# Kernel tuning notes

Measured on AMD Instinct MI355X. Metric: run time of the kernel, lower is better.

The kernel has to match this reference:

```python
import jax, jax.numpy as jnp
import numpy as np
import math

# dims
B, T, HFEAT, E = 32, 8, 128, 128
NUM_CLS, NUM_GLOBAL = 4, 2
NSP = NUM_CLS + NUM_GLOBAL            # 6 special tokens
SCALES = (1, 4, 8)
WINDOW = 4
NHEAD = 8
DH = E // NHEAD                        # 16
NLAYERS = 2                            # blocks per scale = ceil(6/3)
NS = len(SCALES)
F = 512                                # dim_feedforward
ROPE_BASE = 100000.0
NEG = -1e9


def setup_inputs() -> dict:
    key = jax.random.key(0)
    ks = jax.random.split(key, 16)
    def rn(k, shape, s=0.02):
        return jax.random.normal(k, shape, jnp.float32) * s
    inp = {
        'embeddings': jax.random.normal(ks[0], (B, T, NSP + HFEAT, E), jnp.float32),
        'cls_tokens': rn(ks[1], (NUM_CLS, E)),
        'global_tokens': rn(ks[2], (NUM_GLOBAL, E)),
        'Wq': rn(ks[3], (NS, NLAYERS, E, E)),
        'bq': jnp.zeros((NS, NLAYERS, E), jnp.float32),
        'Wk': rn(ks[4], (NS, NLAYERS, E, E)),
        'bk': jnp.zeros((NS, NLAYERS, E), jnp.float32),
        'Wv': rn(ks[5], (NS, NLAYERS, E, E)),
        'bv': jnp.zeros((NS, NLAYERS, E), jnp.float32),
        'Wo': rn(ks[6], (NS, NLAYERS, E, E)),
        'bo': jnp.zeros((NS, NLAYERS, E), jnp.float32),
        'ln1_g': jnp.ones((NS, NLAYERS, E), jnp.float32),
        'ln1_b': jnp.zeros((NS, NLAYERS, E), jnp.float32),
        'ln2_g': jnp.ones((NS, NLAYERS, E), jnp.float32),
        'ln2_b': jnp.zeros((NS, NLAYERS, E), jnp.float32),
        'W1': rn(ks[7], (NS, NLAYERS, E, F)),
        'b1': jnp.zeros((NS, NLAYERS, F), jnp.float32),
        'W2': rn(ks[8], (NS, NLAYERS, F, E)),
        'b2': jnp.zeros((NS, NLAYERS, E), jnp.float32),
        'out_g': jnp.ones((E,), jnp.float32),
        'out_b': jnp.zeros((E,), jnp.float32),
    }
    return inp


def _layernorm(x, g, b, eps=1e-5):
    mu = x.mean(-1, keepdims=True)
    var = ((x - mu) ** 2).mean(-1, keepdims=True)
    return (x - mu) * jax.lax.rsqrt(var + eps) * g + b


def _rope(x):
    # x: (BT, L, H, DH); rotate-half RoPE over head dim
    L = x.shape[1]
    half = DH // 2
    inv = ROPE_BASE ** (-jnp.arange(half, dtype=jnp.float32) / half)
    ang = jnp.arange(L, dtype=jnp.float32)[:, None] * inv[None, :]   # (L, half)
    cos = jnp.cos(ang)[None, :, None, :]
    sin = jnp.sin(ang)[None, :, None, :]
    x1, x2 = x[..., :half], x[..., half:]
    return jnp.concatenate([x1 * cos - x2 * sin, x1 * sin + x2 * cos], axis=-1)


def _sparse_bias(L):
    # global(first NSP) rows/cols fully connected, others window +-WINDOW, diag allowed
    i = jnp.arange(L)
    allowed = (jnp.abs(i[:, None] - i[None, :]) <= WINDOW) | (i[:, None] < NSP) | (i[None, :] < NSP)
    return jnp.where(allowed, 0.0, NEG).astype(jnp.float32)  # (L, L) additive


def _encoder(x, s, Wq, bq, Wk, bk, Wv, bv, Wo, bo, ln1_g, ln1_b, ln2_g, ln2_b, W1, b1, W2, b2, bias):
    # x: (BT, L, E); pre-norm transformer encoder with RoPE attention
    BT, L, _ = x.shape
    for l in range(NLAYERS):
        h = _layernorm(x, ln1_g[s, l], ln1_b[s, l])
        q = (h @ Wq[s, l] + bq[s, l]).reshape(BT, L, NHEAD, DH)
        k = (h @ Wk[s, l] + bk[s, l]).reshape(BT, L, NHEAD, DH)
        v = (h @ Wv[s, l] + bv[s, l]).reshape(BT, L, NHEAD, DH)
        q, k = _rope(q), _rope(k)
        scores = jnp.einsum('blhd,bmhd->bhlm', q, k) / math.sqrt(DH) + bias[None, None]
        attn = jax.nn.softmax(scores, axis=-1)
        o = jnp.einsum('bhlm,bmhd->blhd', attn, v).reshape(BT, L, E)
        x = x + o @ Wo[s, l] + bo[s, l]
        h2 = _layernorm(x, ln2_g[s, l], ln2_b[s, l])
        x = x + jax.nn.gelu(h2 @ W1[s, l] + b1[s, l]) @ W2[s, l] + b2[s, l]
    return x


def reference(embeddings, cls_tokens, global_tokens, Wq, bq, Wk, bk, Wv, bv, Wo, bo,
              ln1_g, ln1_b, ln2_g, ln2_b, W1, b1, W2, b2, out_g, out_b):
    Bb, Tt, HC, Ee = embeddings.shape
    feats = embeddings[..., NSP:, :]                                 # (B,T,H,E)
    specials = jnp.broadcast_to(
        jnp.concatenate([cls_tokens, global_tokens], axis=0)[None, None],
        (Bb, Tt, NSP, Ee))
    cls_per_scale = []
    for s, g in enumerate(SCALES):
        H = feats.shape[2]
        K = H // g  # H divisible by all scales
        grouped = feats.reshape(Bb, Tt, K, g, Ee).mean(axis=3)       # contiguous mean grouping
        seq = jnp.concatenate([specials, grouped], axis=2)           # (B,T,L,E)
        L = NSP + K
        x = seq.reshape(Bb * Tt, L, Ee)
        bias = _sparse_bias(L)
        out = _encoder(x, s, Wq, bq, Wk, bk, Wv, bv, Wo, bo,
                       ln1_g, ln1_b, ln2_g, ln2_b, W1, b1, W2, b2, bias)
        cls_per_scale.append(out.reshape(Bb, Tt, L, Ee)[..., :NUM_CLS, :])
    cls_out = jnp.stack(cls_per_scale, axis=0).mean(axis=0)          # (B,T,num_cls,E)
    cls_out = _layernorm(cls_out, out_g, out_b)
    return cls_out.reshape(Bb, Tt, NUM_CLS * Ee)
```

## Files before the change

### kernel.cpp

```cpp
#include <hip/hip_runtime.h>
#include <hip/hip_bf16.h>

#define BT     256
#define EDIM   128
#define NSP    6
#define RT     49664
#define O1     34304
#define O2     44032
#define KSTR   20

typedef unsigned short u16;
typedef short s16x8 __attribute__((ext_vector_type(8)));
typedef float f32x4 __attribute__((ext_vector_type(4)));

__device__ __forceinline__ float u2f(u16 u){ union{unsigned i; float f;} v; v.i=((unsigned)u)<<16; return v.f; }
__device__ __forceinline__ u16 f2u(float f){
  union{float f; unsigned i;} v; v.f = f;
  unsigned r = v.i + 0x7FFF + ((v.i >> 16) & 1);
  return (u16)(r >> 16);
}
__device__ __forceinline__ float ldin(const void* p, size_t idx, int flag){
  return flag ? u2f(((const u16*)p)[idx]) : ((const float*)p)[idx];
}
__device__ __forceinline__ void unp8(uint4 v, float* f){
  f[0]=u2f((u16)(v.x)); f[1]=u2f((u16)(v.x>>16));
  f[2]=u2f((u16)(v.y)); f[3]=u2f((u16)(v.y>>16));
  f[4]=u2f((u16)(v.z)); f[5]=u2f((u16)(v.z>>16));
  f[6]=u2f((u16)(v.w)); f[7]=u2f((u16)(v.w>>16));
}

__device__ __forceinline__ void rowinfo(int row, int& s, int& r, int& L, int& g){
  if (row < O1){ s=0; r=row;    L=134; g=1; }
  else if (row < O2){ s=1; r=row-O1; L=38; g=4; }
  else { s=2; r=row-O2; L=22; g=8; }
}

__device__ __forceinline__ float gelu_f(float x){
  float u = 1.5957691216f*(x + 0.044715f*x*x*x);
  u = fminf(u, 80.f);
  float w = __expf(u);
  return x * w / (w + 1.f);
}

__global__ void detect_k(const void* ln1g, int* flagp){
  unsigned v = *(const unsigned*)ln1g;
  *flagp = (v == 0x3F803F80u) ? 1 : 0;
}

struct CArg { const void* src; unsigned dstoff; unsigned n; unsigned inblk; unsigned outblk; };
struct CArgs { CArg a[12]; };
__global__ __launch_bounds__(256) void conv_k(CArgs ca, u16* stage, const int* flagp){
  int i = blockIdx.y;
  int flag = *flagp;
  const CArg& c = ca.a[i];
  for (unsigned idx = blockIdx.x*256u + threadIdx.x; idx < c.n; idx += gridDim.x*256u){
    unsigned blk = idx / c.inblk, r = idx % c.inblk;
    float v = flag ? u2f(((const u16*)c.src)[idx]) : ((const float*)c.src)[idx];
    stage[c.dstoff + blk*c.outblk + r] = flag ? ((const u16*)c.src)[idx] : f2u(v);
  }
}

struct WArg { const void* s0; const void* s1; const void* s2; unsigned off; int K; int N; int Nsrc; };
struct WArgs { WArg a[4]; };
__global__ __launch_bounds__(256) void convw_k(WArgs wa, u16* stage, const int* flagp)
{
  int flag = *flagp;
  const WArg& a = wa.a[blockIdx.y];
  const void* srcs[3] = {a.s0, a.s1, a.s2};
  int total = 6 * a.K * a.N;
  u16* dst = stage + a.off;
  for (int idx = blockIdx.x*256 + threadIdx.x; idx < total; idx += gridDim.x*256) {
    int blk = idx / (a.K*a.N);
    int rem = idx % (a.K*a.N);
    int j = rem & 7;
    int t = rem >> 3;
    int n = t % a.N;
    int ck = t / a.N;
    int k = ck*8 + j;
    int w = n / a.Nsrc;
    int nn = n - w*a.Nsrc;
    size_t sidx = (size_t)blk*a.K*a.Nsrc + (size_t)k*a.Nsrc + nn;
    dst[idx] = flag ? ((const u16*)srcs[w])[sidx] : f2u(((const float*)srcs[w])[sidx]);
  }
}

__global__ __launch_bounds__(128) void build_k(const void* __restrict__ emb,
                                               const void* __restrict__ cls,
                                               const void* __restrict__ glob,
                                               float* __restrict__ x,
                                               u16* __restrict__ H,
                                               const u16* __restrict__ lnG,
                                               const u16* __restrict__ lnB,
                                               const int* flagp)
{
  __shared__ float red[4];
  int flag = *flagp;
  int row = blockIdx.x, e = threadIdx.x;
  int s, r, L, g; rowinfo(row, s, r, L, g);
  int seq = r / L, pos = r % L;
  float val;
  if (pos < NSP) {
    val = (pos < 4) ? ldin(cls, pos*EDIM + e, flag) : ldin(glob, (pos-4)*EDIM + e, flag);
  } else {
    int k = pos - NSP;
    size_t base = ((size_t)seq*134 + NSP + (size_t)k*g)*EDIM + e;
    float sum = 0.f;
    for (int j = 0; j < g; j++) sum += ldin(emb, base + (size_t)j*EDIM, flag);
    val = sum / (float)g;
  }
  x[(size_t)row*EDIM + e] = val;
  int wid = e >> 6;
  float sum = val, ss = val*val;
  #pragma unroll
  for (int off = 32; off; off >>= 1) { sum += __shfl_xor(sum, off); ss += __shfl_xor(ss, off); }
  if ((e & 63) == 0) { red[wid] = sum; red[2+wid] = ss; }
  __syncthreads();
  float ts = red[0]+red[1], tss = red[2]+red[3];
  float mu = ts * (1.f/128.f);
  float var = tss * (1.f/128.f) - mu*mu;
  float rs = rsqrtf(var + 1e-5f);
  const u16* gp = lnG + s*2*EDIM;
  const u16* bp = lnB + s*2*EDIM;
  H[(size_t)row*EDIM + e] = f2u((val-mu)*rs*u2f(gp[e]) + u2f(bp[e]));
}

__global__ __launch_bounds__(256) void gemm64_k(
    const u16* __restrict__ A,
    const u16* __restrict__ Wt, const u16* __restrict__ Bias,
    u16* __restrict__ C, int ldc, int N, int layer)
{
  __shared__ u16 As[4][16*136];
  __shared__ u16 Bs[16*128*8];
  const int row0 = blockIdx.x * 64;
  const int n0 = blockIdx.y * 128;
  const int s = row0 < O1 ? 0 : (row0 < O2 ? 1 : 2);
  const u16* Wp = Wt + (size_t)(s*2+layer)*128*N;
  const u16* bp = Bias + (size_t)(s*2+layer)*N + n0;
  const int tid = threadIdx.x;
  const int lane = tid & 63, w = tid >> 6;
  const int g = lane >> 4, l15 = lane & 15;

  #pragma unroll
  for (int i = 0; i < 4; i++) {
    int unit = lane + i*64;
    int r = unit >> 4, kc = unit & 15;
    *(uint4*)&As[w][r*136 + kc*8] = *(const uint4*)(A + (size_t)(row0 + w*16 + r)*128 + kc*8);
  }
  #pragma unroll
  for (int i = 0; i < 8; i++) {
    int u = tid + i*256;
    int kb = u >> 7, nn = u & 127;
    *(uint4*)&Bs[u*8] = *(const uint4*)(Wp + ((size_t)kb*N + n0 + nn)*8);
  }
  __syncthreads();

  f32x4 acc[8];
  #pragma unroll
  for (int nt = 0; nt < 8; nt++) acc[nt] = (f32x4){0.f,0.f,0.f,0.f};
  #pragma unroll
  for (int ks = 0; ks < 4; ks++) {
    int c = ks*4 + g;
    s16x8 af = *(const s16x8*)&As[w][l15*136 + c*8];
    #pragma unroll
    for (int nt = 0; nt < 8; nt++) {
      s16x8 bf = *(const s16x8*)&Bs[(c*128 + nt*16 + l15)*8];
      acc[nt] = __builtin_amdgcn_mfma_f32_16x16x32_bf16(af, bf, acc[nt], 0, 0, 0);
    }
  }

  float bb[8];
  #pragma unroll
  for (int nt = 0; nt < 8; nt++) bb[nt] = u2f(bp[nt*16 + l15]);
  #pragma unroll
  for (int reg = 0; reg < 4; reg++) {
    int row = row0 + w*16 + g*4 + reg;
    #pragma unroll
    for (int nt = 0; nt < 8; nt++)
      C[(size_t)row*ldc + n0 + nt*16 + l15] = f2u(acc[nt][reg] + bb[nt]);
  }
}

template<int LNFUSE>
__global__ __launch_bounds__(256) void wo_ffn_k(
    const u16* __restrict__ O,
    const u16* __restrict__ WOt, const u16* __restrict__ BO,
    const u16* __restrict__ L2G, const u16* __restrict__ L2B,
    const u16* __restrict__ W1t, const u16* __restrict__ B1,
    const u16* __restrict__ W2t, const u16* __restrict__ B2,
    float* __restrict__ X,
    u16* __restrict__ H, const u16* __restrict__ L1G, const u16* __restrict__ L1B,
    int lnidx, int layer)
{
  __shared__ u16 As[64*136];
  __shared__ u16 Ts[64*72];
  __shared__ u16 Bs[8192];
  __shared__ float rsum[64][2];
  __shared__ float rss[64][2];
  const int row0 = blockIdx.x * 64;
  const int s = row0 < O1 ? 0 : (row0 < O2 ? 1 : 2);
  const u16* WOp = WOt + (size_t)(s*2+layer)*16384;
  const u16* bop = BO + (s*2+layer)*128;
  const u16* W1p = W1t + (size_t)(s*2+layer)*65536;
  const u16* b1p = B1 + (s*2+layer)*512;
  const u16* W2p = W2t + (size_t)(s*2+layer)*65536;
  const u16* b2p = B2 + (s*2+layer)*128;
  const int tid = threadIdx.x;
  const int lane = tid & 63, wave = tid >> 6;
  const int g = lane >> 4, l15 = lane & 15;

  #pragma unroll
  for (int i = 0; i < 4; i++) {
    int unit = lane + i*64;
    int r = unit >> 4, kc = unit & 15;
    *(uint4*)&As[(wave*16 + r)*136 + kc*8] = *(const uint4*)(O + (size_t)(row0 + wave*16 + r)*128 + kc*8);
  }
  f32x4 accW[8];
  #pragma unroll
  for (int nt = 0; nt < 8; nt++) accW[nt] = (f32x4){0.f,0.f,0.f,0.f};
  for (int ck = 0; ck < 4; ck++) {
    __syncthreads();
    #pragma unroll
    for (int i = 0; i < 2; i++) {
      int u = tid + i*256;
      *(uint4*)&Bs[u*8] = *(const uint4*)(WOp + ((size_t)(ck*4 + (u>>7))*128 + (u&127))*8);
    }
    __syncthreads();
    s16x8 af = *(const s16x8*)&As[(wave*16 + l15)*136 + (ck*4+g)*8];
    #pragma unroll
    for (int nt = 0; nt < 8; nt++) {
      s16x8 bf = *(const s16x8*)&Bs[(g*128 + nt*16 + l15)*8];
      accW[nt] = __builtin_amdgcn_mfma_f32_16x16x32_bf16(af, bf, accW[nt], 0, 0, 0);
    }
  }
  {
    float bo_[8], gam2[8], bet2[8];
    const u16* g2 = L2G + (s*2+layer)*EDIM;
    const u16* b2l = L2B + (s*2+layer)*EDIM;
    #pragma unroll
    for (int nt = 0; nt < 8; nt++) {
      bo_[nt] = u2f(bop[nt*16+l15]);
      gam2[nt] = u2f(g2[nt*16+l15]);
      bet2[nt] = u2f(b2l[nt*16+l15]);
    }
    #pragma unroll
    for (int reg = 0; reg < 4; reg++) {
      int lr = wave*16 + g*4 + reg;
      int row = row0 + lr;
      float vals[8], ps = 0.f, pss = 0.f;
      #pragma unroll
      for (int nt = 0; nt < 8; nt++) {
        float v = accW[nt][reg] + bo_[nt] + X[(size_t)row*128 + nt*16 + l15];
        vals[nt] = v; ps += v; pss += v*v;
      }
      #pragma unroll
      for (int off = 1; off < 16; off <<= 1) { ps += __shfl_xor(ps, off); pss += __shfl_xor(pss, off); }
      float mu = ps * (1.f/128.f);
      float var = pss * (1.f/128.f) - mu*mu;
      float rs = rsqrtf(var + 1e-5f);
      #pragma unroll
      for (int nt = 0; nt < 8; nt++) {
        X[(size_t)row*128 + nt*16 + l15] = vals[nt];
        As[lr*136 + nt*16 + l15] = f2u((vals[nt]-mu)*rs*gam2[nt] + bet2[nt]);
      }
    }
  }

  const int mw = (wave & 1) * 32;
  const int nw2 = (wave >> 1) * 32;
  const int nwC = (wave >> 1) * 64;

  f32x4 acc2[2][4];
  #pragma unroll
  for (int a = 0; a < 2; a++)
    #pragma unroll
    for (int b = 0; b < 4; b++) acc2[a][b] = (f32x4){0.f,0.f,0.f,0.f};

  for (int f0 = 0; f0 < 512; f0 += 64) {
    __syncthreads();
    #pragma unroll
    for (int i = 0; i < 4; i++) {
      int unit = tid + i*256;
      int nn = unit & 63, kb = unit >> 6;
      *(uint4*)&Bs[(kb*64 + nn)*8] = *(const uint4*)(W1p + ((size_t)kb*512 + f0 + nn)*8);
    }
    __syncthreads();
    f32x4 acc1[2][2];
    #pragma unroll
    for (int a = 0; a < 2; a++)
      #pragma unroll
      for (int b = 0; b < 2; b++) acc1[a][b] = (f32x4){0.f,0.f,0.f,0.f};
    #pragma unroll
    for (int ks = 0; ks < 4; ks++) {
      int c = ks*4 + g;
      s16x8 af[2], bf[2];
      #pragma unroll
      for (int mt = 0; mt < 2; mt++) af[mt] = *(const s16x8*)&As[(mw + mt*16 + l15)*136 + c*8];
      #pragma unroll
      for (int nt = 0; nt < 2; nt++) bf[nt] = *(const s16x8*)&Bs[(c*64 + nw2 + nt*16 + l15)*8];
      #pragma unroll
      for (int mt = 0; mt < 2; mt++)
        #pragma unroll
        for (int nt = 0; nt < 2; nt++)
          acc1[mt][nt] = __builtin_amdgcn_mfma_f32_16x16x32_bf16(af[mt], bf[nt], acc1[mt][nt], 0, 0, 0);
    }
    #pragma unroll
    for (int nt = 0; nt < 2; nt++) {
      float bb1 = u2f(b1p[f0 + nw2 + nt*16 + l15]);
      #pragma unroll
      for (int mt = 0; mt < 2; mt++)
        #pragma unroll
        for (int reg = 0; reg < 4; reg++) {
          int row = mw + mt*16 + g*4 + reg;
          Ts[row*72 + nw2 + nt*16 + l15] = f2u(gelu_f(acc1[mt][nt][reg] + bb1));
        }
    }
    __syncthreads();
    #pragma unroll
    for (int i = 0; i < 4; i++) {
      int unit = tid + i*256;
      int nn = unit & 127, kb = unit >> 7;
      *(uint4*)&Bs[(kb*128 + nn)*8] = *(const uint4*)(W2p + ((size_t)(f0/8 + kb)*128 + nn)*8);
    }
    __syncthreads();
    #pragma unroll
    for (int ks = 0; ks < 2; ks++) {
      int c = ks*4 + g;
      s16x8 af[2], bf[4];
      #pragma unroll
      for (int mt = 0; mt < 2; mt++) af[mt] = *(const s16x8*)&Ts[(mw + mt*16 + l15)*72 + c*8];
      #pragma unroll
      for (int nt = 0; nt < 4; nt++) bf[nt] = *(const s16x8*)&Bs[(c*128 + nwC + nt*16 + l15)*8];
      #pragma unroll
      for (int mt = 0; mt < 2; mt++)
        #pragma unroll
        for (int nt = 0; nt < 4; nt++)
          acc2[mt][nt] = __builtin_amdgcn_mfma_f32_16x16x32_bf16(af[mt], bf[nt], acc2[mt][nt], 0, 0, 0);
    }
  }

  float bb2[4];
  #pragma unroll
  for (int nt = 0; nt < 4; nt++) bb2[nt] = u2f(b2p[nwC + nt*16 + l15]);

  if (LNFUSE) {
    #pragma unroll
    for (int mt = 0; mt < 2; mt++) {
      #pragma unroll
      for (int reg = 0; reg < 4; reg++) {
        int lr = mw + mt*16 + g*4 + reg;
        int row = row0 + lr;
        float ps = 0.f, pss = 0.f;
        #pragma unroll
        for (int nt = 0; nt < 4; nt++) {
          size_t cidx = (size_t)row*128 + nwC + nt*16 + l15;
          float val = acc2[mt][nt][reg] + bb2[nt] + X[cidx];
          acc2[mt][nt][reg] = val;
          ps += val; pss += val*val;
        }
        #pragma unroll
        for (int off = 1; off < 16; off <<= 1) {
          ps += __shfl_xor(ps, off); pss += __shfl_xor(pss, off);
        }
        if (l15 == 0) { rsum[lr][nwC>>6] = ps; rss[lr][nwC>>6] = pss; }
      }
    }
    __syncthreads();
    const u16* gp = L1G + (s*2+lnidx)*EDIM;
    const u16* bpn = L1B + (s*2+lnidx)*EDIM;
    float gam[4], bet[4];
    #pragma unroll
    for (int nt = 0; nt < 4; nt++) { gam[nt] = u2f(gp[nwC+nt*16+l15]); bet[nt] = u2f(bpn[nwC+nt*16+l15]); }
    #pragma unroll
    for (int mt = 0; mt < 2; mt++) {
      #pragma unroll
      for (int reg = 0; reg < 4; reg++) {
        int lr = mw + mt*16 + g*4 + reg;
        int row = row0 + lr;
        float ts = rsum[lr][0]+rsum[lr][1], tss = rss[lr][0]+rss[lr][1];
        float mu = ts * (1.f/128.f);
        float var = tss * (1.f/128.f) - mu*mu;
        float rs = rsqrtf(var + 1e-5f);
        #pragma unroll
        for (int nt = 0; nt < 4; nt++) {
          size_t cidx = (size_t)row*128 + nwC + nt*16 + l15;
          float val = acc2[mt][nt][reg];
          X[cidx] = val;
          H[cidx] = f2u((val-mu)*rs*gam[nt] + bet[nt]);
        }
      }
    }
  } else {
    #pragma unroll
    for (int mt = 0; mt < 2; mt++) {
      #pragma unroll
      for (int reg = 0; reg < 4; reg++) {
        int row = row0 + mw + mt*16 + g*4 + reg;
        #pragma unroll
        for (int nt = 0; nt < 4; nt++) {
          size_t cidx = (size_t)row*128 + nwC + nt*16 + l15;
          X[cidx] += acc2[mt][nt][reg] + bb2[nt];
        }
      }
    }
  }
}

__global__ __launch_bounds__(128) void attn_k(const u16* __restrict__ qkv, u16* __restrict__ o)
{
  __shared__ float Ks[134*KSTR];
  __shared__ float Vs[134*KSTR];
  int gseq = blockIdx.x, hd = blockIdx.y;
  int L, base;
  if (gseq < 256)      { L = 134; base = gseq*134; }
  else if (gseq < 512) { L = 38;  base = O1 + (gseq-256)*38; }
  else                 { L = 22;  base = O2 + (gseq-512)*22; }
  int tid = threadIdx.x;
  for (int u = tid; u < L*2; u += 128) {
    int kv = u & 1, row = u >> 1;
    const u16* p = qkv + (size_t)(base+row)*384 + 128 + kv*128 + hd*16;
    uint4 w0 = *(const uint4*)p, w1 = *(const uint4*)(p+8);
    float f[16];
    unp8(w0, f); unp8(w1, f+8);
    if (kv == 0) {
      #pragma unroll
      for (int d = 0; d < 8; d++) {
        float inv = __expf(-(float)d * (11.512925465f/8.f));
        float ang = (float)row * inv;
        float cs = __cosf(ang), sn = __sinf(ang);
        float a = f[d], b = f[d+8];
        f[d]   = a*cs - b*sn;
        f[d+8] = a*sn + b*cs;
      }
    }
    float* dst = (kv ? Vs : Ks) + row*KSTR;
    #pragma unroll
    for (int d = 0; d < 16; d++) dst[d] = f[d];
  }
  __syncthreads();

  for (int it = tid; it < L - NSP; it += 128) {
    int row = NSP + it;
    const u16* qp = qkv + (size_t)(base+row)*384 + hd*16;
    uint4 w0 = *(const uint4*)qp, w1 = *(const uint4*)(qp+8);
    float q[16]; unp8(w0, q); unp8(w1, q+8);
    #pragma unroll
    for (int d = 0; d < 8; d++) {
      float inv = __expf(-(float)d * (11.512925465f/8.f));
      float ang = (float)row * inv;
      float cs = __cosf(ang), sn = __sinf(ang);
      float a = q[d], b = q[d+8];
      q[d]   = a*cs - b*sn;
      q[d+8] = a*sn + b*cs;
    }
    float m = -1e30f, l = 0.f, oa[16] = {};
    auto step = [&](int j){
      const float4* kr = (const float4*)(Ks + j*KSTR);
      float4 k0 = kr[0], k1 = kr[1], k2 = kr[2], k3 = kr[3];
      float sc = q[0]*k0.x + q[1]*k0.y + q[2]*k0.z + q[3]*k0.w
               + q[4]*k1.x + q[5]*k1.y + q[6]*k1.z + q[7]*k1.w
               + q[8]*k2.x + q[9]*k2.y + q[10]*k2.z + q[11]*k2.w
               + q[12]*k3.x + q[13]*k3.y + q[14]*k3.z + q[15]*k3.w;
      sc *= 0.25f;
      float nm = fmaxf(m, sc);
      float scale = __expf(m - nm);
      float pexp = __expf(sc - nm);
      l = l*scale + pexp;
      const float4* vr = (const float4*)(Vs + j*KSTR);
      float4 v0 = vr[0], v1 = vr[1], v2 = vr[2], v3 = vr[3];
      oa[0]=oa[0]*scale+pexp*v0.x;  oa[1]=oa[1]*scale+pexp*v0.y;
      oa[2]=oa[2]*scale+pexp*v0.z;  oa[3]=oa[3]*scale+pexp*v0.w;
      oa[4]=oa[4]*scale+pexp*v1.x;  oa[5]=oa[5]*scale+pexp*v1.y;
      oa[6]=oa[6]*scale+pexp*v1.z;  oa[7]=oa[7]*scale+pexp*v1.w;
      oa[8]=oa[8]*scale+pexp*v2.x;  oa[9]=oa[9]*scale+pexp*v2.y;
      oa[10]=oa[10]*scale+pexp*v2.z; oa[11]=oa[11]*scale+pexp*v2.w;
      oa[12]=oa[12]*scale+pexp*v3.x; oa[13]=oa[13]*scale+pexp*v3.y;
      oa[14]=oa[14]*scale+pexp*v3.z; oa[15]=oa[15]*scale+pexp*v3.w;
      m = nm;
    };
    #pragma unroll
    for (int j = 0; j < NSP; j++) step(j);
    int jlo = (row-4 > NSP) ? row-4 : NSP;
    int jhi = (row+4 < L-1) ? row+4 : L-1;
    for (int j = jlo; j <= jhi; j++) step(j);
    float invl = 1.f/l;
    u16* op = o + (size_t)(base+row)*EDIM + hd*16;
    #pragma unroll
    for (int d = 0; d < 16; d++) op[d] = f2u(oa[d]*invl);
  }

  if (tid < 96) {
    int row = tid >> 4;
    int u = tid & 15;
    const u16* qp = qkv + (size_t)(base+row)*384 + hd*16;
    uint4 w0 = *(const uint4*)qp, w1 = *(const uint4*)(qp+8);
    float q[16]; unp8(w0, q); unp8(w1, q+8);
    #pragma unroll
    for (int d = 0; d < 8; d++) {
      float inv = __expf(-(float)d * (11.512925465f/8.f));
      float ang = (float)row * inv;
      float cs = __cosf(ang), sn = __sinf(ang);
      float a = q[d], b = q[d+8];
      q[d]   = a*cs - b*sn;
      q[d+8] = a*sn + b*cs;
    }
    float m = -1e30f, l = 0.f, oa[16] = {};
    for (int j = u; j < L; j += 16) {
      const float4* kr = (const float4*)(Ks + j*KSTR);
      float4 k0 = kr[0], k1 = kr[1], k2 = kr[2], k3 = kr[3];
      float sc = q[0]*k0.x + q[1]*k0.y + q[2]*k0.z + q[3]*k0.w
               + q[4]*k1.x + q[5]*k1.y + q[6]*k1.z + q[7]*k1.w
               + q[8]*k2.x + q[9]*k2.y + q[10]*k2.z + q[11]*k2.w
               + q[12]*k3.x + q[13]*k3.y + q[14]*k3.z + q[15]*k3.w;
      sc *= 0.25f;
      float nm = fmaxf(m, sc);
      float scale = __expf(m - nm);
      float pexp = __expf(sc - nm);
      l = l*scale + pexp;
      const float4* vr = (const float4*)(Vs + j*KSTR);
      float4 v0 = vr[0], v1 = vr[1], v2 = vr[2], v3 = vr[3];
      oa[0]=oa[0]*scale+pexp*v0.x;  oa[1]=oa[1]*scale+pexp*v0.y;
      oa[2]=oa[2]*scale+pexp*v0.z;  oa[3]=oa[3]*scale+pexp*v0.w;
      oa[4]=oa[4]*scale+pexp*v1.x;  oa[5]=oa[5]*scale+pexp*v1.y;
      oa[6]=oa[6]*scale+pexp*v1.z;  oa[7]=oa[7]*scale+pexp*v1.w;
      oa[8]=oa[8]*scale+pexp*v2.x;  oa[9]=oa[9]*scale+pexp*v2.y;
      oa[10]=oa[10]*scale+pexp*v2.z; oa[11]=oa[11]*scale+pexp*v2.w;
      oa[12]=oa[12]*scale+pexp*v3.x; oa[13]=oa[13]*scale+pexp*v3.y;
      oa[14]=oa[14]*scale+pexp*v3.z; oa[15]=oa[15]*scale+pexp*v3.w;
      m = nm;
    }
    #pragma unroll
    for (int off = 1; off < 16; off <<= 1) {
      float m2 = __shfl_xor(m, off);
      float l2 = __shfl_xor(l, off);
      float nm = fmaxf(m, m2);
      float s1 = __expf(m - nm), s2 = __expf(m2 - nm);
      #pragma unroll
      for (int d = 0; d < 16; d++) {
        float o2 = __shfl_xor(oa[d], off);
        oa[d] = oa[d]*s1 + o2*s2;
      }
      l = l*s1 + l2*s2;
      m = nm;
    }
    if (u == 0) {
      float invl = 1.f/l;
      u16* op = o + (size_t)(base+row)*EDIM + hd*16;
      #pragma unroll
      for (int d = 0; d < 16; d++) op[d] = f2u(oa[d]*invl);
    }
  }
}

__global__ __launch_bounds__(256) void final_k(const float* __restrict__ x,
                                               const u16* __restrict__ G,
                                               const u16* __restrict__ Bt,
                                               void* __restrict__ out, const int* flagp)
{
  int flag = *flagp;
  int wid = threadIdx.x >> 6, lane = threadIdx.x & 63;
  int idx = blockIdx.x*4 + wid;
  int seq = idx >> 2, c = idx & 3;
  size_t r0 = ((size_t)seq*134 + c)*EDIM;
  size_t r1 = ((size_t)O1 + (size_t)seq*38 + c)*EDIM;
  size_t r2 = ((size_t)O2 + (size_t)seq*22 + c)*EDIM;
  float v0 = (x[r0+lane]    + x[r1+lane]    + x[r2+lane])    * (1.f/3.f);
  float v1 = (x[r0+64+lane] + x[r1+64+lane] + x[r2+64+lane]) * (1.f/3.f);
  float sum = v0 + v1;
  #pragma unroll
  for (int off = 32; off; off >>= 1) sum += __shfl_xor(sum, off);
  float mu = sum * (1.f/128.f);
  float d0 = v0 - mu, d1 = v1 - mu;
  float var = d0*d0 + d1*d1;
  #pragma unroll
  for (int off = 32; off; off >>= 1) var += __shfl_xor(var, off);
  var *= (1.f/128.f);
  float rs = rsqrtf(var + 1e-5f);
  float o0 = d0*rs*u2f(G[lane])    + u2f(Bt[lane]);
  float o1 = d1*rs*u2f(G[64+lane]) + u2f(Bt[64+lane]);
  size_t oi0 = (size_t)seq*512 + c*128 + lane;
  if (flag) { ((u16*)out)[oi0] = f2u(o0); ((u16*)out)[oi0+64] = f2u(o1); }
  else      { ((float*)out)[oi0] = o0;    ((float*)out)[oi0+64] = o1; }
}

#define S_WQKV 0u
#define S_BQKV 294912u
#define S_WO   297216u
#define S_BO   395520u
#define S_W1   396288u
#define S_B1   789504u
#define S_W2   792576u
#define S_B2   1185792u
#define S_L1G  1186560u
#define S_L1B  1187328u
#define S_L2G  1188096u
#define S_L2B  1188864u
#define S_OG   1189632u
#define S_OB   1189760u

extern "C" void kernel_launch(void* const* d_in, const int* in_sizes, int n_in,
                              void* d_out, int out_size, void* d_ws, size_t ws_size,
                              hipStream_t stream) {
  char* wsb = (char*)d_ws;
  int*   flagp = (int*)wsb;
  u16*   stage = (u16*)(wsb + 64);
  float* x     = (float*)(wsb + (size_t)2379840);
  u16*   h     = (u16*)(wsb + (size_t)27807808);
  u16*   qkv   = (u16*)(wsb + (size_t)40521792);

  detect_k<<<1, 1, 0, stream>>>(d_in[11], flagp);

  CArgs ca;
  CArg list[12] = {
    { d_in[4],  S_BQKV,       768, 128, 384 },
    { d_in[6],  S_BQKV+128u,  768, 128, 384 },
    { d_in[8],  S_BQKV+256u,  768, 128, 384 },
    { d_in[10], S_BO,         768, 128, 128 },
    { d_in[16], S_B1,        3072, 512, 512 },
    { d_in[18], S_B2,         768, 128, 128 },
    { d_in[11], S_L1G,        768, 128, 128 },
    { d_in[12], S_L1B,        768, 128, 128 },
    { d_in[13], S_L2G,        768, 128, 128 },
    { d_in[14], S_L2B,        768, 128, 128 },
    { d_in[19], S_OG,         128, 128, 128 },
    { d_in[20], S_OB,         128, 128, 128 },
  };
  for (int i = 0; i < 12; i++) ca.a[i] = list[i];
  conv_k<<<dim3(4, 12), 256, 0, stream>>>(ca, stage, flagp);

  WArgs wa;
  wa.a[0] = { d_in[3],  d_in[5],  d_in[7],  S_WQKV, 128, 384, 128 };
  wa.a[1] = { d_in[9],  d_in[9],  d_in[9],  S_WO,   128, 128, 128 };
  wa.a[2] = { d_in[15], d_in[15], d_in[15], S_W1,   128, 512, 512 };
  wa.a[3] = { d_in[17], d_in[17], d_in[17], S_W2,   512, 128, 128 };
  convw_k<<<dim3(192, 4), 256, 0, stream>>>(wa, stage, flagp);

  build_k<<<RT, 128, 0, stream>>>(d_in[0], d_in[1], d_in[2], x, h, stage+S_L1G, stage+S_L1B, flagp);

  for (int l = 0; l < 2; l++) {
    gemm64_k<<<dim3(RT/64, 3), 256, 0, stream>>>(h, stage+S_WQKV, stage+S_BQKV, qkv, 384, 384, l);
    attn_k<<<dim3(768, 8), 128, 0, stream>>>(qkv, h);
    if (l == 0)
      wo_ffn_k<1><<<RT/64, 256, 0, stream>>>(h, stage+S_WO, stage+S_BO, stage+S_L2G, stage+S_L2B,
                                             stage+S_W1, stage+S_B1, stage+S_W2, stage+S_B2,
                                             x, h, stage+S_L1G, stage+S_L1B, 1, l);
    else
      wo_ffn_k<0><<<RT/64, 256, 0, stream>>>(h, stage+S_WO, stage+S_BO, stage+S_L2G, stage+S_L2B,
                                             stage+S_W1, stage+S_B1, stage+S_W2, stage+S_B2,
                                             x, nullptr, nullptr, nullptr, 0, l);
  }
  final_k<<<BT, 256, 0, stream>>>(x, stage+S_OG, stage+S_OB, d_out, flagp);
}
```

Baseline: 417.5 us.

## Give each wave its own 16-row strip through Wo+FFN, keep residual in registers

The fused Wo+FFN kernel now assigns each wave a full 16-row strip across all output columns instead of a 2x2 wave tiling of 32x32/32x64 tiles. Because a wave owns entire rows, the residual stays in registers (xv) between the attention-output LayerNorm and the FFN output, which removes the intermediate X store and reload. It also removes the shared-memory cross-wave LayerNorm reduction and its barrier. In exchange, B fragments from shared memory are no longer reused across two M tiles, so LDS reads per MFMA rise, and register pressure goes up from the 32-float residual array plus 8 accumulators.

Result: slower. 428.8 us (+2.7%).

```diff
diff --git a/kernel.cpp b/kernel.cpp
--- a/kernel.cpp
+++ b/kernel.cpp
@@ -191,11 +191,9 @@
     u16* __restrict__ H, const u16* __restrict__ L1G, const u16* __restrict__ L1B,
     int lnidx, int layer)
 {
-  __shared__ u16 As[64*136];
-  __shared__ u16 Ts[64*72];
+  __shared__ u16 As[4][16*136];
+  __shared__ u16 Ts[4][16*72];
   __shared__ u16 Bs[8192];
-  __shared__ float rsum[64][2];
-  __shared__ float rss[64][2];
   const int row0 = blockIdx.x * 64;
   const int s = row0 < O1 ? 0 : (row0 < O2 ? 1 : 2);
   const u16* WOp = WOt + (size_t)(s*2+layer)*16384;
@@ -205,14 +203,14 @@
   const u16* W2p = W2t + (size_t)(s*2+layer)*65536;
   const u16* b2p = B2 + (s*2+layer)*128;
   const int tid = threadIdx.x;
-  const int lane = tid & 63, wave = tid >> 6;
+  const int lane = tid & 63, w = tid >> 6;
   const int g = lane >> 4, l15 = lane & 15;
 
   #pragma unroll
   for (int i = 0; i < 4; i++) {
     int unit = lane + i*64;
     int r = unit >> 4, kc = unit & 15;
-    *(uint4*)&As[(wave*16 + r)*136 + kc*8] = *(const uint4*)(O + (size_t)(row0 + wave*16 + r)*128 + kc*8);
+    *(uint4*)&As[w][r*136 + kc*8] = *(const uint4*)(O + (size_t)(row0 + w*16 + r)*128 + kc*8);
   }
   f32x4 accW[8];
   #pragma unroll
@@ -225,13 +223,14 @@
       *(uint4*)&Bs[u*8] = *(const uint4*)(WOp + ((size_t)(ck*4 + (u>>7))*128 + (u&127))*8);
     }
     __syncthreads();
-    s16x8 af = *(const s16x8*)&As[(wave*16 + l15)*136 + (ck*4+g)*8];
+    s16x8 af = *(const s16x8*)&As[w][l15*136 + (ck*4+g)*8];
     #pragma unroll
     for (int nt = 0; nt < 8; nt++) {
       s16x8 bf = *(const s16x8*)&Bs[(g*128 + nt*16 + l15)*8];
       accW[nt] = __builtin_amdgcn_mfma_f32_16x16x32_bf16(af, bf, accW[nt], 0, 0, 0);
     }
   }
+  float xv[4][8];
   {
     float bo_[8], gam2[8], bet2[8];
     const u16* g2 = L2G + (s*2+layer)*EDIM;
@@ -244,13 +243,12 @@
     }
     #pragma unroll
     for (int reg = 0; reg < 4; reg++) {
-      int lr = wave*16 + g*4 + reg;
-      int row = row0 + lr;
-      float vals[8], ps = 0.f, pss = 0.f;
+      int row = row0 + w*16 + g*4 + reg;
+      float ps = 0.f, pss = 0.f;
       #pragma unroll
       for (int nt = 0; nt < 8; nt++) {
         float v = accW[nt][reg] + bo_[nt] + X[(size_t)row*128 + nt*16 + l15];
-        vals[nt] = v; ps += v; pss += v*v;
+        xv[reg][nt] = v; ps += v; pss += v*v;
       }
       #pragma unroll
       for (int off = 1; off < 16; off <<= 1) { ps += __shfl_xor(ps, off); pss += __shfl_xor(pss, off); }
@@ -258,22 +256,14 @@
       float var = pss * (1.f/128.f) - mu*mu;
       float rs = rsqrtf(var + 1e-5f);
       #pragma unroll
-      for (int nt = 0; nt < 8; nt++) {
-        X[(size_t)row*128 + nt*16 + l15] = vals[nt];
-        As[lr*136 + nt*16 + l15] = f2u((vals[nt]-mu)*rs*gam2[nt] + bet2[nt]);
-      }
-    }
-  }
-
-  const int mw = (wave & 1) * 32;
-  const int nw2 = (wave >> 1) * 32;
-  const int nwC = (wave >> 1) * 64;
-
-  f32x4 acc2[2][4];
-  #pragma unroll
-  for (int a = 0; a < 2; a++)
-    #pragma unroll
-    for (int b = 0; b < 4; b++) acc2[a][b] = (f32x4){0.f,0.f,0.f,0.f};
+      for (int nt = 0; nt < 8; nt++)
+        As[w][(g*4+reg)*136 + nt*16 + l15] = f2u((xv[reg][nt]-mu)*rs*gam2[nt] + bet2[nt]);
+    }
+  }
+
+  f32x4 acc2[8];
+  #pragma unroll
+  for (int nt = 0; nt < 8; nt++) acc2[nt] = (f32x4){0.f,0.f,0.f,0.f};
 
   for (int f0 = 0; f0 < 512; f0 += 64) {
     __syncthreads();
@@ -284,35 +274,25 @@
       *(uint4*)&Bs[(kb*64 + nn)*8] = *(const uint4*)(W1p + ((size_t)kb*512 + f0 + nn)*8);
     }
     __syncthreads();
-    f32x4 acc1[2][2];
-    #pragma unroll
-    for (int a = 0; a < 2; a++)
-      #pragma unroll
-      for (int b = 0; b < 2; b++) acc1[a][b] = (f32x4){0.f,0.f,0.f,0.f};
+    f32x4 acc1[4];
+    #pragma unroll
+    for (int nt = 0; nt < 4; nt++) acc1[nt] = (f32x4){0.f,0.f,0.f,0.f};
     #pragma unroll
     for (int ks = 0; ks < 4; ks++) {
       int c = ks*4 + g;
-      s16x8 af[2], bf[2];
-      #pragma unroll
-      for (int mt = 0; mt < 2; mt++) af[mt] = *(const s16x8*)&As[(mw + mt*16 + l15)*136 + c*8];
-      #pragma unroll
-      for (int nt = 0; nt < 2; nt++) bf[nt] = *(const s16x8*)&Bs[(c*64 + nw2 + nt*16 + l15)*8];
-      #pragma unroll
-      for (int mt = 0; mt < 2; mt++)
-        #pragma unroll
-        for (int nt = 0; nt < 2; nt++)
-          acc1[mt][nt] = __builtin_amdgcn_mfma_f32_16x16x32_bf16(af[mt], bf[nt], acc1[mt][nt], 0, 0, 0);
-    }
-    #pragma unroll
-    for (int nt = 0; nt < 2; nt++) {
-      float bb1 = u2f(b1p[f0 + nw2 + nt*16 + l15]);
-      #pragma unroll
-      for (int mt = 0; mt < 2; mt++)
-        #pragma unroll
-        for (int reg = 0; reg < 4; reg++) {
-          int row = mw + mt*16 + g*4 + reg;
-          Ts[row*72 + nw2 + nt*16 + l15] = f2u(gelu_f(acc1[mt][nt][reg] + bb1));
-        }
+      s16x8 af = *(const s16x8*)&As[w][l15*136 + c*8];
+      #pragma unroll
+      for (int nt = 0; nt < 4; nt++) {
+        s16x8 bf = *(const s16x8*)&Bs[(c*64 + nt*16 + l15)*8];
+        acc1[nt] = __builtin_amdgcn_mfma_f32_16x16x32_bf16(af, bf, acc1[nt], 0, 0, 0);
+      }
+    }
+    #pragma unroll
+    for (int nt = 0; nt < 4; nt++) {
+      float bb1 = u2f(b1p[f0 + nt*16 + l15]);
+      #pragma unroll
+      for (int reg = 0; reg < 4; reg++)
+        Ts[w][(g*4+reg)*72 + nt*16 + l15] = f2u(gelu_f(acc1[nt][reg] + bb1));
     }
     __syncthreads();
     #pragma unroll
@@ -325,82 +305,53 @@
     #pragma unroll
     for (int ks = 0; ks < 2; ks++) {
       int c = ks*4 + g;
-      s16x8 af[2], bf[4];
-      #pragma unroll
-      for (int mt = 0; mt < 2; mt++) af[mt] = *(const s16x8*)&Ts[(mw + mt*16 + l15)*72 + c*8];
-      #pragma unroll
-      for (int nt = 0; nt < 4; nt++) bf[nt] = *(const s16x8*)&Bs[(c*128 + nwC + nt*16 + l15)*8];
-      #pragma unroll
-      for (int mt = 0; mt < 2; mt++)
-        #pragma unroll
-        for (int nt = 0; nt < 4; nt++)
-          acc2[mt][nt] = __builtin_amdgcn_mfma_f32_16x16x32_bf16(af[mt], bf[nt], acc2[mt][nt], 0, 0, 0);
-    }
-  }
-
-  float bb2[4];
-  #pragma unroll
-  for (int nt = 0; nt < 4; nt++) bb2[nt] = u2f(b2p[nwC + nt*16 + l15]);
+      s16x8 af2 = *(const s16x8*)&Ts[w][l15*72 + c*8];
+      #pragma unroll
+      for (int nt = 0; nt < 8; nt++) {
+        s16x8 bf = *(const s16x8*)&Bs[(c*128 + nt*16 + l15)*8];
+        acc2[nt] = __builtin_amdgcn_mfma_f32_16x16x32_bf16(af2, bf, acc2[nt], 0, 0, 0);
+      }
+    }
+  }
+
+  float bb2[8];
+  #pragma unroll
+  for (int nt = 0; nt < 8; nt++) bb2[nt] = u2f(b2p[nt*16 + l15]);
 
   if (LNFUSE) {
-    #pragma unroll
-    for (int mt = 0; mt < 2; mt++) {
-      #pragma unroll
-      for (int reg = 0; reg < 4; reg++) {
-        int lr = mw + mt*16 + g*4 + reg;
-        int row = row0 + lr;
-        float ps = 0.f, pss = 0.f;
-        #pragma unroll
-        for (int nt = 0; nt < 4; nt++) {
-          size_t cidx = (size_t)row*128 + nwC + nt*16 + l15;
-          float val = acc2[mt][nt][reg] + bb2[nt] + X[cidx];
-          acc2[mt][nt][reg] = val;
-          ps += val; pss += val*val;
-        }
-        #pragma unroll
-        for (int off = 1; off < 16; off <<= 1) {
-          ps += __shfl_xor(ps, off); pss += __shfl_xor(pss, off);
-        }
-        if (l15 == 0) { rsum[lr][nwC>>6] = ps; rss[lr][nwC>>6] = pss; }
-      }
-    }
-    __syncthreads();
+    float gam[8], bet[8];
     const u16* gp = L1G + (s*2+lnidx)*EDIM;
     const u16* bpn = L1B + (s*2+lnidx)*EDIM;
-    float gam[4], bet[4];
-    #pragma unroll
-    for (int nt = 0; nt < 4; nt++) { gam[nt] = u2f(gp[nwC+nt*16+l15]); bet[nt] = u2f(bpn[nwC+nt*16+l15]); }
-    #pragma unroll
-    for (int mt = 0; mt < 2; mt++) {
-      #pragma unroll
-      for (int reg = 0; reg < 4; reg++) {
-        int lr = mw + mt*16 + g*4 + reg;
-        int row = row0 + lr;
-        float ts = rsum[lr][0]+rsum[lr][1], tss = rss[lr][0]+rss[lr][1];
-        float mu = ts * (1.f/128.f);
-        float var = tss * (1.f/128.f) - mu*mu;
-        float rs = rsqrtf(var + 1e-5f);
-        #pragma unroll
-        for (int nt = 0; nt < 4; nt++) {
-          size_t cidx = (size_t)row*128 + nwC + nt*16 + l15;
-          float val = acc2[mt][nt][reg];
-          X[cidx] = val;
-          H[cidx] = f2u((val-mu)*rs*gam[nt] + bet[nt]);
-        }
+    #pragma unroll
+    for (int nt = 0; nt < 8; nt++) { gam[nt] = u2f(gp[nt*16+l15]); bet[nt] = u2f(bpn[nt*16+l15]); }
+    #pragma unroll
+    for (int reg = 0; reg < 4; reg++) {
+      int row = row0 + w*16 + g*4 + reg;
+      float ps = 0.f, pss = 0.f;
+      #pragma unroll
+      for (int nt = 0; nt < 8; nt++) {
+        float v = acc2[nt][reg] + bb2[nt] + xv[reg][nt];
+        xv[reg][nt] = v; ps += v; pss += v*v;
       }
+      #pragma unroll
+      for (int off = 1; off < 16; off <<= 1) { ps += __shfl_xor(ps, off); pss += __shfl_xor(pss, off); }
+      float mu = ps * (1.f/128.f);
+      float var = pss * (1.f/128.f) - mu*mu;
+      float rs = rsqrtf(var + 1e-5f);
+      #pragma unroll
+      for (int nt = 0; nt < 8; nt++) {
+        size_t cidx = (size_t)row*128 + nt*16 + l15;
+        X[cidx] = xv[reg][nt];
+        H[cidx] = f2u((xv[reg][nt]-mu)*rs*gam[nt] + bet[nt]);
+      }
     }
   } else {
     #pragma unroll
-    for (int mt = 0; mt < 2; mt++) {
-      #pragma unroll
-      for (int reg = 0; reg < 4; reg++) {
-        int row = row0 + mw + mt*16 + g*4 + reg;
-        #pragma unroll
-        for (int nt = 0; nt < 4; nt++) {
-          size_t cidx = (size_t)row*128 + nwC + nt*16 + l15;
-          X[cidx] += acc2[mt][nt][reg] + bb2[nt];
-        }
-      }
+    for (int reg = 0; reg < 4; reg++) {
+      int row = row0 + w*16 + g*4 + reg;
+      #pragma unroll
+      for (int nt = 0; nt < 8; nt++)
+        X[(size_t)row*128 + nt*16 + l15] = acc2[nt][reg] + bb2[nt] + xv[reg][nt];
     }
   }
 }
```
